# Kernel tuning notes

Hardware: AMD Instinct MI355X
Metric: run time of the kernel (lower is better)

The kernel has to match this reference:

```python
import jax, jax.numpy as jnp
import numpy as np

N = 65536   # collocation points
D = 2       # input dim
C = 16      # num subdomains / partitions (4x4 grid)
PH = 128    # PoU hidden dim
PNMID = 2   # PoU middle (residual) layers: depth=4 -> 2 middle
SW = 256    # subnet width
SNMID = 2   # subnet middle layers: eqx MLP depth=3 -> 2 width->width layers


def setup_inputs() -> dict:
    key = jax.random.key(0)
    ks = jax.random.split(key, 8)

    def w(k, shape, fan_in):
        return jax.random.normal(k, shape, jnp.float32) / jnp.sqrt(jnp.float32(fan_in))

    x = jax.random.uniform(ks[0], (N, D), jnp.float32)  # points in [0,1]^2
    # 4x4 grid of axis-aligned subdomains covering [0,1]^2
    g = np.linspace(0.0, 1.0, 5)
    lo = np.stack(np.meshgrid(g[:-1], g[:-1], indexing='ij'), -1).reshape(-1, 2)
    hi = np.stack(np.meshgrid(g[1:], g[1:], indexing='ij'), -1).reshape(-1, 2)
    centers = jnp.asarray((lo + hi) / 2.0, jnp.float32)  # [C, D]
    scales = jnp.asarray((hi - lo) / 2.0, jnp.float32)   # [C, D]

    return dict(
        x=x, centers=centers, scales=scales,
        pou_W0=w(ks[1], (D, PH), D), pou_b0=jnp.zeros((PH,), jnp.float32),
        pou_Wmid=w(ks[2], (PNMID, PH, PH), PH), pou_bmid=jnp.zeros((PNMID, PH), jnp.float32),
        pou_Wl=w(ks[3], (PH, C), PH), pou_bl=jnp.zeros((C,), jnp.float32),
        sub_W0=w(ks[4], (C, D, SW), D), sub_b0=jnp.zeros((C, SW), jnp.float32),
        sub_Wmid=w(ks[5], (C, SNMID, SW, SW), SW), sub_bmid=jnp.zeros((C, SNMID, SW), jnp.float32),
        sub_Wl=w(ks[6], (C, SW, 1), SW), sub_bl=jnp.zeros((C, 1), jnp.float32),
    )


def reference(x, centers, scales,
              pou_W0, pou_b0, pou_Wmid, pou_bmid, pou_Wl, pou_bl,
              sub_W0, sub_b0, sub_Wmid, sub_bmid, sub_Wl, sub_bl):
    # --- PoU gating net: residual ReLU MLP + softmax over partitions ---
    h = jax.nn.relu(x @ pou_W0 + pou_b0)                  # [N, PH]
    for l in range(pou_Wmid.shape[0]):
        h = h + jax.nn.relu(h @ pou_Wmid[l] + pou_bmid[l])
    wgt = jax.nn.softmax(h @ pou_Wl + pou_bl, axis=-1)    # [N, C] window weights

    # --- per-subdomain input normalization + batched subnet MLPs (tanh) ---
    xn = (x[None, :, :] - centers[:, None, :]) / scales[:, None, :]  # [C, N, D]
    g = jnp.tanh(jnp.einsum('cnd,cdw->cnw', xn, sub_W0) + sub_b0[:, None, :])  # [C, N, SW]
    for l in range(sub_Wmid.shape[1]):
        g = jnp.tanh(jnp.einsum('cnw,cwv->cnv', g, sub_Wmid[:, l]) + sub_bmid[:, l][:, None, :])
    u = (jnp.einsum('cnw,cwo->cno', g, sub_Wl) + sub_bl[:, None, :])[:, :, 0]  # [C, N]

    # --- windowed weighted sum:  acc_n = sum_c w[n,c] * u[c,n] ---
    acc = jnp.einsum('nc,cn->n', wgt, u)                  # [N]

    # --- ansatz: hard Dirichlet BC on the unit box: u = acc * prod_d x_d (1-x_d) ---
    return acc * jnp.prod(x * (1.0 - x), axis=-1)
```

## Files before the change

kernel.cpp:

```cpp
#include <hip/hip_runtime.h>

#define NPTS 65536
#define CC 16
#define PH 128
#define SW 256
#define MB 64
#define SP 264

typedef _Float16 half8 __attribute__((ext_vector_type(8)));
typedef _Float16 half4 __attribute__((ext_vector_type(4)));
typedef _Float16 half2 __attribute__((ext_vector_type(2)));
typedef float float4_ __attribute__((ext_vector_type(4)));
typedef float float2_ __attribute__((ext_vector_type(2)));

__device__ __forceinline__ float fast_tanh(float x) {
    float e = __builtin_amdgcn_exp2f(x * 2.8853900817779268f);
    float r = __builtin_amdgcn_rcpf(e + 1.0f);
    return fmaf(-2.0f, r, 1.0f);
}

__device__ __forceinline__ half4 pack4(float a, float b, float c, float d) {
    half2 lo = __builtin_bit_cast(half2, __builtin_amdgcn_cvt_pkrtz(a, b));
    half2 hi = __builtin_bit_cast(half2, __builtin_amdgcn_cvt_pkrtz(c, d));
    half4 h;
    h[0] = lo[0]; h[1] = lo[1]; h[2] = hi[0]; h[3] = hi[1];
    return h;
}

__global__ __launch_bounds__(256) void prep_wt(const float* __restrict__ Wmid,
                                               _Float16* __restrict__ Wt) {
    __shared__ float T[64][65];
    int b = blockIdx.x;
    int cl = b >> 4;
    int tile = b & 15;
    int w0 = (tile >> 2) * 64, v0 = (tile & 3) * 64;
    int t = threadIdx.x;
    int col = t & 63, row4 = t >> 6;
    const float* src = Wmid + ((size_t)cl << 16);
#pragma unroll
    for (int rr = 0; rr < 16; ++rr) {
        int wl = rr * 4 + row4;
        T[wl][col] = src[(size_t)(w0 + wl) * 256 + v0 + col];
    }
    __syncthreads();
    _Float16* dst = Wt + ((size_t)cl << 16);
#pragma unroll
    for (int rr = 0; rr < 16; ++rr) {
        int v = rr * 4 + row4;
        dst[(size_t)(v0 + v) * 256 + w0 + col] = (_Float16)T[col][v];
    }
}

__global__ __launch_bounds__(256) void pou_kernel(
    const float* __restrict__ x, const float* __restrict__ W0,
    const float* __restrict__ b0, const float* __restrict__ Wmid,
    const float* __restrict__ bmid, const float* __restrict__ Wl,
    const float* __restrict__ bl, float* __restrict__ wgtT) {
    __shared__ float hA[64][PH + 1];
    int t = threadIdx.x;
    int p = t & 63;
    int g4 = __builtin_amdgcn_readfirstlane(t >> 6);
    int jb = g4 * 32;
    int n0 = blockIdx.x * 64;
    float x0 = x[(size_t)(n0 + p) * 2];
    float x1 = x[(size_t)(n0 + p) * 2 + 1];

#pragma unroll
    for (int jj = 0; jj < 32; ++jj) {
        int j = jb + jj;
        float a = x0 * W0[j] + x1 * W0[PH + j] + b0[j];
        hA[p][j] = a > 0.f ? a : 0.f;
    }
    __syncthreads();

    for (int l = 0; l < 2; ++l) {
        float acc[32];
#pragma unroll
        for (int jj = 0; jj < 32; ++jj) acc[jj] = bmid[l * PH + jb + jj];
        for (int k = 0; k < PH; ++k) {
            float hv = hA[p][k];
#pragma unroll
            for (int jj = 0; jj < 32; ++jj)
                acc[jj] += hv * Wmid[(l * PH + k) * PH + jb + jj];
        }
        float resv[32];
#pragma unroll
        for (int jj = 0; jj < 32; ++jj) resv[jj] = hA[p][jb + jj];
        __syncthreads();
#pragma unroll
        for (int jj = 0; jj < 32; ++jj) {
            float r = acc[jj] > 0.f ? acc[jj] : 0.f;
            hA[p][jb + jj] = resv[jj] + r;
        }
        __syncthreads();
    }

    int c4 = g4 * 4;
    float lacc[4];
#pragma unroll
    for (int cc = 0; cc < 4; ++cc) lacc[cc] = bl[c4 + cc];
    for (int k = 0; k < PH; ++k) {
        float hv = hA[p][k];
#pragma unroll
        for (int cc = 0; cc < 4; ++cc) lacc[cc] += hv * Wl[k * CC + c4 + cc];
    }
    __syncthreads();
#pragma unroll
    for (int cc = 0; cc < 4; ++cc) hA[p][c4 + cc] = lacc[cc];
    __syncthreads();

    if (t < 64) {
        float lg[CC];
#pragma unroll
        for (int c = 0; c < CC; ++c) lg[c] = hA[t][c];
        float m = lg[0];
#pragma unroll
        for (int c = 1; c < CC; ++c) m = fmaxf(m, lg[c]);
        float s = 0.f;
#pragma unroll
        for (int c = 0; c < CC; ++c) {
            lg[c] = __builtin_amdgcn_exp2f((lg[c] - m) * 1.4426950408889634f);
            s += lg[c];
        }
        float inv = 1.0f / s;
#pragma unroll
        for (int c = 0; c < CC; ++c)
            wgtT[(size_t)c * NPTS + n0 + t] = lg[c] * inv;
    }
}

__global__ __launch_bounds__(256, 4) void subnet_kernel(
    const float* __restrict__ x, const float* __restrict__ centers,
    const float* __restrict__ scales, const float* __restrict__ W0,
    const float* __restrict__ b0, const _Float16* __restrict__ Wt,
    const float* __restrict__ bmid, const float* __restrict__ Wl,
    const float* __restrict__ bl, const float* __restrict__ wgtT,
    float* __restrict__ out) {
    __shared__ _Float16 g[MB * SP];
    __shared__ float part[4][MB];
    int t = threadIdx.x;
    int c = blockIdx.y;
    int n0 = blockIdx.x * MB;

    {
        float cx0 = centers[c * 2], cx1 = centers[c * 2 + 1];
        float is0 = 1.0f / scales[c * 2], is1 = 1.0f / scales[c * 2 + 1];
        int ln = t & 63;
        int pb = (t >> 6) * 16;
        const float* W0c = W0 + (size_t)c * 2 * SW;
        float4_ w0 = *(const float4_*)&W0c[ln * 4];
        float4_ w1 = *(const float4_*)&W0c[SW + ln * 4];
        float4_ bb = *(const float4_*)&b0[c * SW + ln * 4];
#pragma unroll 4
        for (int p = 0; p < 16; ++p) {
            float2_ xv = *(const float2_*)&x[(size_t)(n0 + pb + p) * 2];
            float xn0 = (xv[0] - cx0) * is0;
            float xn1 = (xv[1] - cx1) * is1;
            float tv[4];
#pragma unroll
            for (int j = 0; j < 4; ++j)
                tv[j] = fast_tanh(fmaf(xn0, w0[j], fmaf(xn1, w1[j], bb[j])));
            *(half4*)&g[(pb + p) * SP + ln * 4] = pack4(tv[0], tv[1], tv[2], tv[3]);
        }
    }
    __syncthreads();

    int lane = t & 63;
    int wave = t >> 6;
    int quad = lane >> 4;
    int l16 = lane & 15;
    int mb = wave * 64;

    {
        const _Float16* Wp = Wt + (((size_t)(c * 2 + 0)) << 16);
        const _Float16* Arow = Wp + (mb + l16) * SW + quad * 8;
        const float* bp = bmid + (c * 2 + 0) * SW + mb + quad * 4;
        float4_ acc[4][4];
#pragma unroll
        for (int mt = 0; mt < 4; ++mt) {
            float4_ bv = *(const float4_*)&bp[mt * 16];
#pragma unroll
            for (int nt = 0; nt < 4; ++nt) acc[mt][nt] = bv;
        }
#pragma unroll
        for (int kt = 0; kt < 8; ++kt) {
            half8 a[4], b[4];
#pragma unroll
            for (int mt = 0; mt < 4; ++mt)
                a[mt] = *(const half8*)&Arow[mt * 16 * SW + kt * 32];
#pragma unroll
            for (int nt = 0; nt < 4; ++nt)
                b[nt] = *(const half8*)&g[(nt * 16 + l16) * SP + kt * 32 + quad * 8];
#pragma unroll
            for (int mt = 0; mt < 4; ++mt)
#pragma unroll
                for (int nt = 0; nt < 4; ++nt)
                    acc[mt][nt] = __builtin_amdgcn_mfma_f32_16x16x32_f16(
                        a[mt], b[nt], acc[mt][nt], 0, 0, 0);
        }
        __syncthreads();
#pragma unroll
        for (int mt = 0; mt < 4; ++mt) {
#pragma unroll
            for (int nt = 0; nt < 4; ++nt) {
                float t0 = fast_tanh(acc[mt][nt][0]);
                float t1 = fast_tanh(acc[mt][nt][1]);
                float t2 = fast_tanh(acc[mt][nt][2]);
                float t3 = fast_tanh(acc[mt][nt][3]);
                *(half4*)&g[(nt * 16 + l16) * SP + mb + mt * 16 + quad * 4] =
                    pack4(t0, t1, t2, t3);
            }
        }
        __syncthreads();
    }

    {
        const _Float16* Wp = Wt + (((size_t)(c * 2 + 1)) << 16);
        const _Float16* Arow = Wp + (mb + l16) * SW + quad * 8;
        const float* bp = bmid + (c * 2 + 1) * SW + mb + quad * 4;
        float4_ acc[4][4];
#pragma unroll
        for (int mt = 0; mt < 4; ++mt) {
            float4_ bv = *(const float4_*)&bp[mt * 16];
#pragma unroll
            for (int nt = 0; nt < 4; ++nt) acc[mt][nt] = bv;
        }
#pragma unroll
        for (int kt = 0; kt < 8; ++kt) {
            half8 a[4], b[4];
#pragma unroll
            for (int mt = 0; mt < 4; ++mt)
                a[mt] = *(const half8*)&Arow[mt * 16 * SW + kt * 32];
#pragma unroll
            for (int nt = 0; nt < 4; ++nt)
                b[nt] = *(const half8*)&g[(nt * 16 + l16) * SP + kt * 32 + quad * 8];
#pragma unroll
            for (int mt = 0; mt < 4; ++mt)
#pragma unroll
                for (int nt = 0; nt < 4; ++nt)
                    acc[mt][nt] = __builtin_amdgcn_mfma_f32_16x16x32_f16(
                        a[mt], b[nt], acc[mt][nt], 0, 0, 0);
        }
        const float* wlp = Wl + c * SW + mb + quad * 4;
        float s[4] = {0.f, 0.f, 0.f, 0.f};
#pragma unroll
        for (int mt = 0; mt < 4; ++mt) {
            float4_ wv = *(const float4_*)&wlp[mt * 16];
#pragma unroll
            for (int nt = 0; nt < 4; ++nt) {
                float t0 = fast_tanh(acc[mt][nt][0]);
                float t1 = fast_tanh(acc[mt][nt][1]);
                float t2 = fast_tanh(acc[mt][nt][2]);
                float t3 = fast_tanh(acc[mt][nt][3]);
                s[nt] += fmaf(t0, wv[0],
                          fmaf(t1, wv[1], fmaf(t2, wv[2], t3 * wv[3])));
            }
        }
#pragma unroll
        for (int nt = 0; nt < 4; ++nt) {
            s[nt] += __shfl_xor(s[nt], 16);
            s[nt] += __shfl_xor(s[nt], 32);
        }
        if (quad == 0) {
#pragma unroll
            for (int nt = 0; nt < 4; ++nt) part[wave][nt * 16 + l16] = s[nt];
        }
    }
    __syncthreads();
    if (t < MB) {
        int n = n0 + t;
        float uv = part[0][t] + part[1][t] + part[2][t] + part[3][t] + bl[c];
        float w = wgtT[(size_t)c * NPTS + n];
        float2_ xv = *(const float2_*)&x[(size_t)n * 2];
        float ans = (xv[0] * (1.f - xv[0])) * (xv[1] * (1.f - xv[1]));
        atomicAdd(&out[n], uv * w * ans);
    }
}

extern "C" void kernel_launch(void* const* d_in, const int* in_sizes, int n_in,
                              void* d_out, int out_size, void* d_ws, size_t ws_size,
                              hipStream_t stream) {
    const float* x = (const float*)d_in[0];
    const float* centers = (const float*)d_in[1];
    const float* scales = (const float*)d_in[2];
    const float* pou_W0 = (const float*)d_in[3];
    const float* pou_b0 = (const float*)d_in[4];
    const float* pou_Wmid = (const float*)d_in[5];
    const float* pou_bmid = (const float*)d_in[6];
    const float* pou_Wl = (const float*)d_in[7];
    const float* pou_bl = (const float*)d_in[8];
    const float* sub_W0 = (const float*)d_in[9];
    const float* sub_b0 = (const float*)d_in[10];
    const float* sub_Wmid = (const float*)d_in[11];
    const float* sub_bmid = (const float*)d_in[12];
    const float* sub_Wl = (const float*)d_in[13];
    const float* sub_bl = (const float*)d_in[14];
    float* out = (float*)d_out;

    _Float16* wt = (_Float16*)d_ws;
    float* wgtT = (float*)((char*)d_ws + (4u << 20));

    hipMemsetAsync(out, 0, (size_t)out_size * sizeof(float), stream);
    prep_wt<<<dim3(512), dim3(256), 0, stream>>>(sub_Wmid, wt);
    pou_kernel<<<dim3(NPTS / 64), dim3(256), 0, stream>>>(
        x, pou_W0, pou_b0, pou_Wmid, pou_bmid, pou_Wl, pou_bl, wgtT);
    subnet_kernel<<<dim3(NPTS / MB, CC), dim3(256), 0, stream>>>(
        x, centers, scales, sub_W0, sub_b0, wt, sub_bmid, sub_Wl, sub_bl,
        wgtT, out);
}
```

Measured before the change: 644.4 us.

## Fold tanh exp2 scale into weights and run first subnet layer on MFMA

Pre-multiplies the mid-layer and first-layer weights and biases by 2/ln2 during weight prep, so the tanh no longer needs a per-element multiply. The first subnet layer (K=2) is recast as an MFMA with its K dimension zero-padded to 32 instead of scalar FMAs per point. This removes VALU work from the tanh-heavy epilogues. The cost is an extra prep kernel, fp16 rounding of the scaled first-layer inputs and weights, and more shared memory.

```diff
diff --git a/kernel.cpp b/kernel.cpp
--- a/kernel.cpp
+++ b/kernel.cpp
@@ -6,6 +6,8 @@
 #define SW 256
 #define MB 64
 #define SP 264
+#define SPX 40
+#define TSC 2.8853900817779268f
 
 typedef _Float16 half8 __attribute__((ext_vector_type(8)));
 typedef _Float16 half4 __attribute__((ext_vector_type(4)));
@@ -13,8 +15,8 @@
 typedef float float4_ __attribute__((ext_vector_type(4)));
 typedef float float2_ __attribute__((ext_vector_type(2)));
 
-__device__ __forceinline__ float fast_tanh(float x) {
-    float e = __builtin_amdgcn_exp2f(x * 2.8853900817779268f);
+__device__ __forceinline__ float fast_tanh_pre(float a) {
+    float e = __builtin_amdgcn_exp2f(a);
     float r = __builtin_amdgcn_rcpf(e + 1.0f);
     return fmaf(-2.0f, r, 1.0f);
 }
@@ -47,8 +49,30 @@
 #pragma unroll
     for (int rr = 0; rr < 16; ++rr) {
         int v = rr * 4 + row4;
-        dst[(size_t)(v0 + v) * 256 + w0 + col] = (_Float16)T[col][v];
-    }
+        dst[(size_t)(v0 + v) * 256 + w0 + col] = (_Float16)(T[col][v] * TSC);
+    }
+}
+
+__global__ __launch_bounds__(256) void prep_small(
+    const float* __restrict__ W0, const float* __restrict__ b0,
+    const float* __restrict__ bmid, _Float16* __restrict__ W0t,
+    float* __restrict__ b0s, float* __restrict__ bmids) {
+    int c = blockIdx.x;
+    int w = threadIdx.x;
+    float w0v = W0[(c * 2 + 0) * SW + w] * TSC;
+    float w1v = W0[(c * 2 + 1) * SW + w] * TSC;
+    _Float16* dst = W0t + (((size_t)c * SW + w) << 5);
+    half8 z = {};
+    half8 v = {};
+    v[0] = (_Float16)w0v;
+    v[1] = (_Float16)w1v;
+    *(half8*)&dst[0] = v;
+    *(half8*)&dst[8] = z;
+    *(half8*)&dst[16] = z;
+    *(half8*)&dst[24] = z;
+    b0s[c * SW + w] = b0[c * SW + w] * TSC;
+    bmids[(c * 2 + 0) * SW + w] = bmid[(c * 2 + 0) * SW + w] * TSC;
+    bmids[(c * 2 + 1) * SW + w] = bmid[(c * 2 + 1) * SW + w] * TSC;
 }
 
 __global__ __launch_bounds__(256) void pou_kernel(
@@ -131,37 +155,32 @@
 
 __global__ __launch_bounds__(256, 4) void subnet_kernel(
     const float* __restrict__ x, const float* __restrict__ centers,
-    const float* __restrict__ scales, const float* __restrict__ W0,
-    const float* __restrict__ b0, const _Float16* __restrict__ Wt,
-    const float* __restrict__ bmid, const float* __restrict__ Wl,
+    const float* __restrict__ scales, const _Float16* __restrict__ W0t,
+    const float* __restrict__ b0s, const _Float16* __restrict__ Wt,
+    const float* __restrict__ bmids, const float* __restrict__ Wl,
     const float* __restrict__ bl, const float* __restrict__ wgtT,
     float* __restrict__ out) {
     __shared__ _Float16 g[MB * SP];
+    __shared__ _Float16 gx[MB * SPX];
     __shared__ float part[4][MB];
     int t = threadIdx.x;
     int c = blockIdx.y;
     int n0 = blockIdx.x * MB;
 
     {
-        float cx0 = centers[c * 2], cx1 = centers[c * 2 + 1];
-        float is0 = 1.0f / scales[c * 2], is1 = 1.0f / scales[c * 2 + 1];
-        int ln = t & 63;
-        int pb = (t >> 6) * 16;
-        const float* W0c = W0 + (size_t)c * 2 * SW;
-        float4_ w0 = *(const float4_*)&W0c[ln * 4];
-        float4_ w1 = *(const float4_*)&W0c[SW + ln * 4];
-        float4_ bb = *(const float4_*)&b0[c * SW + ln * 4];
-#pragma unroll 4
-        for (int p = 0; p < 16; ++p) {
-            float2_ xv = *(const float2_*)&x[(size_t)(n0 + pb + p) * 2];
-            float xn0 = (xv[0] - cx0) * is0;
-            float xn1 = (xv[1] - cx1) * is1;
-            float tv[4];
-#pragma unroll
-            for (int j = 0; j < 4; ++j)
-                tv[j] = fast_tanh(fmaf(xn0, w0[j], fmaf(xn1, w1[j], bb[j])));
-            *(half4*)&g[(pb + p) * SP + ln * 4] = pack4(tv[0], tv[1], tv[2], tv[3]);
-        }
+        int p = t >> 2, j4 = t & 3;
+        half8 v = {};
+        if (j4 == 0) {
+            float cx0 = centers[c * 2], cx1 = centers[c * 2 + 1];
+            float is0 = 1.0f / scales[c * 2], is1 = 1.0f / scales[c * 2 + 1];
+            float2_ xv = *(const float2_*)&x[(size_t)(n0 + p) * 2];
+            half2 xn = __builtin_bit_cast(
+                half2, __builtin_amdgcn_cvt_pkrtz((xv[0] - cx0) * is0,
+                                                  (xv[1] - cx1) * is1));
+            v[0] = xn[0];
+            v[1] = xn[1];
+        }
+        *(half8*)&gx[p * SPX + j4 * 8] = v;
     }
     __syncthreads();
 
@@ -172,9 +191,47 @@
     int mb = wave * 64;
 
     {
+        const _Float16* Arow = W0t + (((size_t)c * SW + mb + l16) << 5) + quad * 8;
+        const float* bp = b0s + c * SW + mb + quad * 4;
+        float4_ acc[4][4];
+#pragma unroll
+        for (int mt = 0; mt < 4; ++mt) {
+            float4_ bv = *(const float4_*)&bp[mt * 16];
+#pragma unroll
+            for (int nt = 0; nt < 4; ++nt) acc[mt][nt] = bv;
+        }
+        half8 a[4], b[4];
+#pragma unroll
+        for (int mt = 0; mt < 4; ++mt)
+            a[mt] = *(const half8*)&Arow[mt * 16 * 32];
+#pragma unroll
+        for (int nt = 0; nt < 4; ++nt)
+            b[nt] = *(const half8*)&gx[(nt * 16 + l16) * SPX + quad * 8];
+#pragma unroll
+        for (int mt = 0; mt < 4; ++mt)
+#pragma unroll
+            for (int nt = 0; nt < 4; ++nt)
+                acc[mt][nt] = __builtin_amdgcn_mfma_f32_16x16x32_f16(
+                    a[mt], b[nt], acc[mt][nt], 0, 0, 0);
+#pragma unroll
+        for (int mt = 0; mt < 4; ++mt) {
+#pragma unroll
+            for (int nt = 0; nt < 4; ++nt) {
+                float t0 = fast_tanh_pre(acc[mt][nt][0]);
+                float t1 = fast_tanh_pre(acc[mt][nt][1]);
+                float t2 = fast_tanh_pre(acc[mt][nt][2]);
+                float t3 = fast_tanh_pre(acc[mt][nt][3]);
+                *(half4*)&g[(nt * 16 + l16) * SP + mb + mt * 16 + quad * 4] =
+                    pack4(t0, t1, t2, t3);
+            }
+        }
+        __syncthreads();
+    }
+
+    {
         const _Float16* Wp = Wt + (((size_t)(c * 2 + 0)) << 16);
         const _Float16* Arow = Wp + (mb + l16) * SW + quad * 8;
-        const float* bp = bmid + (c * 2 + 0) * SW + mb + quad * 4;
+        const float* bp = bmids + (c * 2 + 0) * SW + mb + quad * 4;
         float4_ acc[4][4];
 #pragma unroll
         for (int mt = 0; mt < 4; ++mt) {
@@ -203,10 +260,10 @@
         for (int mt = 0; mt < 4; ++mt) {
 #pragma unroll
             for (int nt = 0; nt < 4; ++nt) {
-                float t0 = fast_tanh(acc[mt][nt][0]);
-                float t1 = fast_tanh(acc[mt][nt][1]);
-                float t2 = fast_tanh(acc[mt][nt][2]);
-                float t3 = fast_tanh(acc[mt][nt][3]);
+                float t0 = fast_tanh_pre(acc[mt][nt][0]);
+                float t1 = fast_tanh_pre(acc[mt][nt][1]);
+                float t2 = fast_tanh_pre(acc[mt][nt][2]);
+                float t3 = fast_tanh_pre(acc[mt][nt][3]);
                 *(half4*)&g[(nt * 16 + l16) * SP + mb + mt * 16 + quad * 4] =
                     pack4(t0, t1, t2, t3);
             }
@@ -217,7 +274,7 @@
     {
         const _Float16* Wp = Wt + (((size_t)(c * 2 + 1)) << 16);
         const _Float16* Arow = Wp + (mb + l16) * SW + quad * 8;
-        const float* bp = bmid + (c * 2 + 1) * SW + mb + quad * 4;
+        const float* bp = bmids + (c * 2 + 1) * SW + mb + quad * 4;
         float4_ acc[4][4];
 #pragma unroll
         for (int mt = 0; mt < 4; ++mt) {
@@ -248,10 +305,10 @@
             float4_ wv = *(const float4_*)&wlp[mt * 16];
 #pragma unroll
             for (int nt = 0; nt < 4; ++nt) {
-                float t0 = fast_tanh(acc[mt][nt][0]);
-                float t1 = fast_tanh(acc[mt][nt][1]);
-                float t2 = fast_tanh(acc[mt][nt][2]);
-                float t3 = fast_tanh(acc[mt][nt][3]);
+                float t0 = fast_tanh_pre(acc[mt][nt][0]);
+                float t1 = fast_tanh_pre(acc[mt][nt][1]);
+                float t2 = fast_tanh_pre(acc[mt][nt][2]);
+                float t3 = fast_tanh_pre(acc[mt][nt][3]);
                 s[nt] += fmaf(t0, wv[0],
                           fmaf(t1, wv[1], fmaf(t2, wv[2], t3 * wv[3])));
             }
@@ -297,14 +354,19 @@
     const float* sub_bl = (const float*)d_in[14];
     float* out = (float*)d_out;
 
-    _Float16* wt = (_Float16*)d_ws;
-    float* wgtT = (float*)((char*)d_ws + (4u << 20));
+    char* ws = (char*)d_ws;
+    _Float16* wt = (_Float16*)ws;
+    float* wgtT = (float*)(ws + (4u << 20));
+    _Float16* w0t = (_Float16*)(ws + (8u << 20));
+    float* b0s = (float*)(ws + (8u << 20) + 262144);
+    float* bmids = (float*)(ws + (8u << 20) + 278528);
 
     hipMemsetAsync(out, 0, (size_t)out_size * sizeof(float), stream);
     prep_wt<<<dim3(512), dim3(256), 0, stream>>>(sub_Wmid, wt);
+    prep_small<<<dim3(CC), dim3(256), 0, stream>>>(sub_W0, sub_b0, sub_bmid,
+                                                   w0t, b0s, bmids);
     pou_kernel<<<dim3(NPTS / 64), dim3(256), 0, stream>>>(
         x, pou_W0, pou_b0, pou_Wmid, pou_bmid, pou_Wl, pou_bl, wgtT);
     subnet_kernel<<<dim3(NPTS / MB, CC), dim3(256), 0, stream>>>(
-        x, centers, scales, sub_W0, sub_b0, wt, sub_bmid, sub_Wl, sub_bl,
-        wgtT, out);
-}
+        x, centers, scales, w0t, b0s, wt, bmids, sub_Wl, sub_bl, wgtT, out);
+}
```

Result: slower. 693.2 us (+7.6%).
